# Kernel optimization log

Hardware: AMD Instinct MI355X
Metric: run time of the kernel (lower is better)

## Reference

```python
import jax, jax.numpy as jnp
import numpy as np

N = 20000      # atoms
E = 320000     # edges
G = 16         # graphs
NEL = 4        # chemical elements
M0 = 64        # 0e channels
M1 = 32        # 1o channels
NB = 8         # Bessel basis
L = 2          # conv layers
HID = 64       # radial MLP hidden
RMAX = 4.0
RIN = RMAX - 0.5
NNB = 16.0     # n_neighbors normalization


def _bessel(r):
    # Bessel radial embedding with smooth cosine cutoff between RIN and RMAX
    r_safe = jnp.maximum(r, 1e-6)
    n = jnp.arange(1, NB + 1, dtype=r.dtype)
    f = jnp.sqrt(2.0 / RMAX) * jnp.sin(n[None, :] * jnp.pi * r_safe[:, None] / RMAX) / r_safe[:, None]
    t = (r - RIN) / (RMAX - RIN)
    env = jnp.where(r < RIN, 1.0, jnp.where(r > RMAX, 0.0, 0.5 * (jnp.cos(jnp.pi * t) + 1.0)))
    return f * env[:, None]


def _conv(s, v, attrs, sh0, sh1, src, dst, remb, Wscs, Wscv, W1s, W1v, R0, R1, R2, W2s, W2v):
    # self-connection: FC tensor product of node features with scalar species attrs
    sc_s = jnp.einsum('ni,ne,ieo->no', s, attrs, Wscs) / np.sqrt(M0 * NEL)    # [N, M0+M1]
    sc_v = jnp.einsum('nic,ne,ieo->noc', v, attrs, Wscv) / np.sqrt(M1 * NEL)  # [N, M1, 3]
    # irrep-wise linear (channel mixing)
    s1 = s @ W1s / np.sqrt(M0)
    v1 = jnp.einsum('nic,io->noc', v, W1v) / np.sqrt(M1)
    # gather to edges
    se, ve = s1[src], v1[src]
    # radial MLP -> per-edge tensor-product weights (2*M0 + 2*M1 = 192)
    w = jax.nn.silu(remb @ R0 / np.sqrt(NB))
    w = jax.nn.silu(w @ R1 / np.sqrt(HID))
    w = w @ R2 / np.sqrt(HID)
    w1, w2, w3, w4 = w[:, :M0], w[:, M0:2 * M0], w[:, 2 * M0:2 * M0 + M1], w[:, 2 * M0 + M1:]
    # CG tensor product paths (uvu): 0e*0e->0e, 1o*1o->0e, 0e*1o->1o, 1o*0e->1o
    m_s = jnp.concatenate([
        w1 * se * sh0[:, None],
        w4 * jnp.einsum('eic,ec->ei', ve, sh1) / np.sqrt(3.0),
    ], axis=1)                                                   # [E, M0+M1]
    m_v = jnp.concatenate([
        (w2 * se)[:, :, None] * sh1[:, None, :],
        (w3 * sh0[:, None])[:, :, None] * ve,
    ], axis=1)                                                   # [E, M0+M1, 3]
    # scatter-sum aggregation
    a_s = jax.ops.segment_sum(m_s, dst, num_segments=N) / np.sqrt(NNB)
    a_v = jax.ops.segment_sum(m_v, dst, num_segments=N) / np.sqrt(NNB)
    # linear back to hidden irreps (+ gate scalars) and self-connection
    o_s = a_s @ W2s / np.sqrt(M0 + M1) + sc_s                    # [N, M0+M1]
    o_v = jnp.einsum('nic,io->noc', a_v, W2v) / np.sqrt(M0 + M1) + sc_v
    # gate nonlinearity: silu on scalars, silu-gates on vectors
    gate = jax.nn.silu(o_s[:, M0:])
    return jax.nn.silu(o_s[:, :M0]), o_v * gate[:, :, None]


def _forward(nodes, dR, senders, receivers, n_node, W_embed, W_sc_s, W_sc_v, W_l1_s, W_l1_v,
             Wr0, Wr1, Wr2, W_l2_s, W_l2_v, W_en1, W_en2, W_mag1, W_mag2,
             scale_occ, shift_occ, energy_scale, energy_shift):
    r = jnp.linalg.norm(dR, axis=-1)
    u = dR / jnp.maximum(r, 1e-6)[:, None]
    sh0 = jnp.ones_like(r)                 # Y0 (component norm)
    sh1 = np.sqrt(3.0) * u                 # Y1 (component norm)
    remb = _bessel(r)                      # [E, NB]
    s = nodes @ W_embed / np.sqrt(NEL)     # initial scalar embedding
    v = jnp.zeros((N, M1, 3), dtype=s.dtype)
    for l in range(L):
        s, v = _conv(s, v, nodes, sh0, sh1, senders, receivers, remb,
                     W_sc_s[l], W_sc_v[l], W_l1_s[l], W_l1_v[l],
                     Wr0[l], Wr1[l], Wr2[l], W_l2_s[l], W_l2_v[l])
    # energy readout
    h_en = s @ W_en1 / np.sqrt(M0)
    atomic = h_en @ W_en2 / np.sqrt(M0 // 2)
    atomic = energy_scale * atomic + energy_shift
    gidx = jnp.repeat(jnp.arange(G), n_node, total_repeat_length=N)
    energy = jax.ops.segment_sum(atomic, gidx, num_segments=G)   # [G, 1]
    # magnetization readout
    h_mag = s @ W_mag1 / np.sqrt(M0)
    mags = h_mag @ W_mag2 / np.sqrt(M0 // 2)                     # [N, 2]
    mags = (nodes[:, :-1] @ scale_occ) * mags + (nodes[:, :-1] @ shift_occ)
    return energy, mags


def setup_inputs() -> dict:
    key = jax.random.key(0)
    ks = jax.random.split(key, 30)
    f = jnp.float32
    inp = {
        'nodes': jax.random.uniform(ks[0], (N, NEL), dtype=f),
        'dR': jax.random.normal(ks[1], (E, 3), dtype=f),
        'senders': jax.random.randint(ks[2], (E,), 0, N, dtype=jnp.int32),
        'receivers': jax.random.randint(ks[3], (E,), 0, N, dtype=jnp.int32),
        'n_node': jnp.full((G,), N // G, dtype=jnp.int32),
        'W_embed': jax.random.normal(ks[4], (NEL, M0), dtype=f),
        'W_sc_s': jax.random.normal(ks[5], (L, M0, NEL, M0 + M1), dtype=f),
        'W_sc_v': jax.random.normal(ks[6], (L, M1, NEL, M1), dtype=f),
        'W_l1_s': jax.random.normal(ks[7], (L, M0, M0), dtype=f),
        'W_l1_v': jax.random.normal(ks[8], (L, M1, M1), dtype=f),
        'Wr0': jax.random.normal(ks[9], (L, NB, HID), dtype=f),
        'Wr1': jax.random.normal(ks[10], (L, HID, HID), dtype=f),
        'Wr2': jax.random.normal(ks[11], (L, HID, 2 * M0 + 2 * M1), dtype=f),
        'W_l2_s': jax.random.normal(ks[12], (L, M0 + M1, M0 + M1), dtype=f),
        'W_l2_v': jax.random.normal(ks[13], (L, M0 + M1, M1), dtype=f),
        'W_en1': jax.random.normal(ks[14], (M0, M0 // 2), dtype=f),
        'W_en2': jax.random.normal(ks[15], (M0 // 2, 1), dtype=f),
        'W_mag1': jax.random.normal(ks[16], (M0, M0 // 2), dtype=f),
        'W_mag2': jax.random.normal(ks[17], (M0 // 2, 2), dtype=f),
        'scale_occ': jax.random.uniform(ks[18], (NEL - 1, 2), dtype=f),
        'shift_occ': jax.random.normal(ks[19], (NEL - 1, 2), dtype=f),
        'energy_scale': jnp.ones((), dtype=f),
        'energy_shift': jnp.zeros((), dtype=f),
    }
    return inp


def reference(nodes, dR, senders, receivers, n_node, W_embed, W_sc_s, W_sc_v, W_l1_s, W_l1_v,
              Wr0, Wr1, Wr2, W_l2_s, W_l2_v, W_en1, W_en2, W_mag1, W_mag2,
              scale_occ, shift_occ, energy_scale, energy_shift):
    return _forward(nodes, dR, senders, receivers, n_node, W_embed, W_sc_s, W_sc_v, W_l1_s, W_l1_v,
                    Wr0, Wr1, Wr2, W_l2_s, W_l2_v, W_en1, W_en2, W_mag1, W_mag2,
                    scale_occ, shift_occ, energy_scale, energy_shift)
```

## Files before the change

### kernel.cpp

```cpp
#include <hip/hip_runtime.h>
#include <hip/hip_fp16.h>
#include <math.h>

#define NN 20000
#define NE 320000
#define NG 16
#define ECAP 48

typedef _Float16 f16x2 __attribute__((ext_vector_type(2)));
typedef _Float16 f16x8 __attribute__((ext_vector_type(8)));
typedef float    f32x4 __attribute__((ext_vector_type(4)));

__device__ __forceinline__ float dot2f(f16x2 a, f16x2 b, float c){
#if defined(__has_builtin)
#if __has_builtin(__builtin_amdgcn_fdot2)
  return __builtin_amdgcn_fdot2(a, b, c, false);
#else
  return c + (float)a.x*(float)b.x + (float)a.y*(float)b.y;
#endif
#else
  return c + (float)a.x*(float)b.x + (float)a.y*(float)b.y;
#endif
}

__device__ __forceinline__ f16x2 pack2f(float a, float b){
  f16x2 r; r.x = (_Float16)a; r.y = (_Float16)b; return r;
}

__device__ __forceinline__ float silu_f(float x){ return x / (1.0f + __expf(-x)); }

__device__ __forceinline__ void bessel8(const float* __restrict__ dR, int e, float* rb){
  float x = dR[3*e+0], y = dR[3*e+1], z = dR[3*e+2];
  float r = sqrtf(x*x + y*y + z*z);
  float rs = fmaxf(r, 1e-6f);
  float inv = 1.0f / rs;
  float env;
  if (r < 3.5f) env = 1.0f;
  else if (r > 4.0f) env = 0.0f;
  else {
    float t = (r - 3.5f) * 2.0f;
    env = 0.5f * (cosf(3.14159265358979323846f * t) + 1.0f);
  }
  float c = 0.7071067811865476f * inv * env;
  #pragma unroll
  for (int k=0;k<8;k++){
    float arg = (float)(k+1) * 0.7853981633974483f * rs;
    rb[k] = c * sinf(arg);
  }
}

__global__ void k_geom(const float* __restrict__ dR, float* __restrict__ sh1){
  int e = blockIdx.x*256 + threadIdx.x;
  if (e >= NE) return;
  float x = dR[3*e+0], y = dR[3*e+1], z = dR[3*e+2];
  float r = sqrtf(x*x + y*y + z*z);
  float inv = 1.0f / fmaxf(r, 1e-6f);
  const float SQ3 = 1.7320508075688772f;
  sh1[3*e+0] = SQ3 * x * inv;
  sh1[3*e+1] = SQ3 * y * inv;
  sh1[3*e+2] = SQ3 * z * inv;
}

__global__ void k_prep(const float* __restrict__ dR, const int* __restrict__ senders,
                       const int* __restrict__ perm,
                       float* __restrict__ sh1, float* __restrict__ dRp,
                       int* __restrict__ sendp){
  int p = blockIdx.x*256 + threadIdx.x;
  if (p >= NE) return;
  int e = perm[p];
  float x = dR[3*e+0], y = dR[3*e+1], z = dR[3*e+2];
  dRp[3*p+0] = x; dRp[3*p+1] = y; dRp[3*p+2] = z;
  float r = sqrtf(x*x + y*y + z*z);
  float inv = 1.0f / fmaxf(r, 1e-6f);
  const float SQ3 = 1.7320508075688772f;
  sh1[3*p+0] = SQ3 * x * inv;
  sh1[3*p+1] = SQ3 * y * inv;
  sh1[3*p+2] = SQ3 * z * inv;
  sendp[p] = senders[e];
}

__global__ void k_wt(const float* __restrict__ Wscs, const float* __restrict__ Wscv,
                     float* __restrict__ Wst, float* __restrict__ Wvt){
  int idx = blockIdx.x*256 + threadIdx.x;
  if (idx < 49152){
    int l = idx/24576, r = idx - l*24576;
    int i = r/384; int rem = r - i*384; int e = rem/96; int o = rem - e*96;
    Wst[l*24576 + i*384 + o*4 + e] = Wscs[idx];
  } else if (idx < 49152 + 8192){
    int k = idx - 49152;
    int l = k/4096, r = k - l*4096;
    int i = r/128; int rem = r - i*128; int e = rem/32; int op = rem - e*32;
    Wvt[l*4096 + i*128 + op*4 + e] = Wscv[idx];
  }
}

__global__ void k_embed(const float* __restrict__ nodes, const float* __restrict__ W,
                        float* __restrict__ s){
  int idx = blockIdx.x*256 + threadIdx.x;
  int n = idx>>6, o = idx&63;
  float a = nodes[n*4+0]*W[o] + nodes[n*4+1]*W[64+o]
          + nodes[n*4+2]*W[128+o] + nodes[n*4+3]*W[192+o];
  s[idx] = 0.5f*a;
}

__global__ void k_hist(const int* __restrict__ receivers, int* __restrict__ cnt){
  int e = blockIdx.x*256 + threadIdx.x;
  if (e < NE) atomicAdd(&cnt[receivers[e]], 1);
}

__global__ void k_scan(const int* __restrict__ cnt, int* __restrict__ row, int* __restrict__ cur){
  __shared__ int lsum[1024];
  int t = threadIdx.x;
  int base = t*20;
  int local[20];
  int s = 0;
  #pragma unroll
  for (int i=0;i<20;i++){
    int idx = base+i;
    int v = (idx<NN) ? cnt[idx] : 0;
    local[i] = s; s += v;
  }
  lsum[t] = s; __syncthreads();
  for (int off=1; off<1024; off<<=1){
    int v = (t>=off) ? lsum[t-off] : 0;
    __syncthreads();
    lsum[t] += v;
    __syncthreads();
  }
  int pre = (t>0) ? lsum[t-1] : 0;
  #pragma unroll
  for (int i=0;i<20;i++){
    int idx = base+i;
    if (idx<NN){ int r = pre+local[i]; row[idx]=r; cur[idx]=r; }
  }
  if (t==1023) row[NN] = lsum[1023];
}

__global__ void k_scatter(const int* __restrict__ receivers, int* __restrict__ cur,
                          int* __restrict__ perm){
  int e = blockIdx.x*256 + threadIdx.x;
  if (e < NE){
    int d = receivers[e];
    int p = atomicAdd(&cur[d], 1);
    perm[p] = e;
  }
}

__global__ void k_node(const float* __restrict__ s, const float* __restrict__ v,
                       const float* __restrict__ attrs,
                       const float* __restrict__ W1s, const float* __restrict__ W1v,
                       const float* __restrict__ Wscst, const float* __restrict__ Wscvt,
                       __half* __restrict__ s1, __half* __restrict__ v1,
                       float* __restrict__ scs, float* __restrict__ scv){
  __shared__ float ls[16][64];
  __shared__ float lv[16][96];
  __shared__ float la[16][4];
  int tid = threadIdx.x;
  int nb = blockIdx.x*16;
  for (int i=tid;i<1024;i+=256) ls[i>>6][i&63] = s[(size_t)(nb+(i>>6))*64 + (i&63)];
  for (int i=tid;i<1536;i+=256){ int j=i/96, q=i-96*j; lv[j][q] = v[(size_t)(nb+j)*96+q]; }
  if (tid<64) la[tid>>2][tid&3] = attrs[(nb+(tid>>2))*4 + (tid&3)];
  __syncthreads();
  int w = tid>>6, q = tid&63;
  int jb = w*4;
  float laj[4][4];
  #pragma unroll
  for (int j=0;j<4;j++)
    #pragma unroll
    for (int e=0;e<4;e++) laj[j][e] = la[jb+j][e];

  {
    float acc[4] = {0,0,0,0};
    for (int i=0;i<64;i++){
      float wv = W1s[i*64+q];
      #pragma unroll
      for (int j=0;j<4;j++) acc[j] = fmaf(ls[jb+j][i], wv, acc[j]);
    }
    #pragma unroll
    for (int j=0;j<4;j++) s1[(size_t)(nb+jb+j)*64+q] = __float2half(acc[j]*0.125f);
  }
  #pragma unroll 1
  for (int o=q;o<96;o+=64){
    float t0[4]={0,0,0,0}, t1[4]={0,0,0,0}, t2[4]={0,0,0,0}, t3[4]={0,0,0,0};
    for (int i=0;i<64;i++){
      float4 wv4 = *(const float4*)(Wscst + i*384 + o*4);
      #pragma unroll
      for (int j=0;j<4;j++){
        float sv = ls[jb+j][i];
        t0[j] = fmaf(sv, wv4.x, t0[j]);
        t1[j] = fmaf(sv, wv4.y, t1[j]);
        t2[j] = fmaf(sv, wv4.z, t2[j]);
        t3[j] = fmaf(sv, wv4.w, t3[j]);
      }
    }
    #pragma unroll
    for (int j=0;j<4;j++){
      float acc = t0[j]*laj[j][0] + t1[j]*laj[j][1]
                + t2[j]*laj[j][2] + t3[j]*laj[j][3];
      scs[(size_t)(nb+jb+j)*96+o] = acc*0.0625f;
    }
  }
  #pragma unroll 1
  for (int f=q;f<96;f+=64){
    int op=f/3, c=f-3*op;
    float acc[4] = {0,0,0,0};
    for (int i=0;i<32;i++){
      float wv = W1v[i*32+op];
      #pragma unroll
      for (int j=0;j<4;j++) acc[j] = fmaf(lv[jb+j][i*3+c], wv, acc[j]);
    }
    #pragma unroll
    for (int j=0;j<4;j++) v1[(size_t)(nb+jb+j)*96+f] = __float2half(acc[j]*0.17677669529663687f);
  }
  #pragma unroll 1
  for (int f=q;f<96;f+=64){
    int op=f/3, c=f-3*op;
    float t0[4]={0,0,0,0}, t1[4]={0,0,0,0}, t2[4]={0,0,0,0}, t3[4]={0,0,0,0};
    for (int i=0;i<32;i++){
      float4 wv4 = *(const float4*)(Wscvt + i*128 + op*4);
      #pragma unroll
      for (int j=0;j<4;j++){
        float vv = lv[jb+j][i*3+c];
        t0[j] = fmaf(vv, wv4.x, t0[j]);
        t1[j] = fmaf(vv, wv4.y, t1[j]);
        t2[j] = fmaf(vv, wv4.z, t2[j]);
        t3[j] = fmaf(vv, wv4.w, t3[j]);
      }
    }
    #pragma unroll
    for (int j=0;j<4;j++){
      float acc = t0[j]*laj[j][0] + t1[j]*laj[j][1]
                + t2[j]*laj[j][2] + t3[j]*laj[j][3];
      scv[(size_t)(nb+jb+j)*96+f] = acc*0.08838834764831845f;
    }
  }
}

#define R2S 196
#define HT2S 68
__launch_bounds__(256, 4)
__global__ void k_edgew(const float* __restrict__ dRp,
                        const int* __restrict__ row, int n0, int n1, int cap,
                        const float* __restrict__ R0, const float* __restrict__ R1,
                        const float* __restrict__ R2,
                        __half* __restrict__ wbuf){
  __shared__ __align__(16) f16x2 hT2[32*HT2S];
  __shared__ __align__(16) float r0s[512];
  __shared__ __align__(16) f16x2 wgt2[32*R2S];
  int tid = threadIdx.x;
  int p0 = row[n0], p1 = row[n1];
  int vmax = p1 - p0; if (vmax > cap) vmax = cap;
  int tbase = blockIdx.x*64;
  if (tbase >= vmax) return;
  int vcnt = vmax - tbase; if (vcnt > 64) vcnt = 64;

  if (tid < 128) ((float4*)r0s)[tid] = ((const float4*)R0)[tid];
  for (int i=tid; i<2048; i+=256){
    int kp = i>>6, j = i&63;
    wgt2[kp*HT2S + j] = pack2f(R1[(2*kp)*64 + j], R1[(2*kp+1)*64 + j]);
  }
  float* hTf = (float*)hT2;
  if (tid < 64){
    float rbv[8];
    if (tid < vcnt){
      bessel8(dRp, p0 + tbase + tid, rbv);
    } else {
      #pragma unroll
      for (int k=0;k<8;k++) rbv[k]=0.0f;
    }
    #pragma unroll
    for (int k=0;k<8;k++) hTf[k*HT2S + tid] = rbv[k];
  }
  __syncthreads();

  int eg = tid & 15;
  int jg = tid >> 4, j0 = jg*4;

  float rb[8][4];
  {
    const float4* hTf4 = (const float4*)hTf;
    #pragma unroll
    for (int k=0;k<8;k++){
      float4 v = hTf4[k*17 + eg];
      rb[k][0]=v.x; rb[k][1]=v.y; rb[k][2]=v.z; rb[k][3]=v.w;
    }
  }
  float a[4][4];
  #pragma unroll
  for (int j=0;j<4;j++)
    #pragma unroll
    for (int e=0;e<4;e++) a[j][e]=0.0f;
  {
    const float4* r0s4 = (const float4*)r0s;
    #pragma unroll
    for (int k=0;k<8;k++){
      float4 w = r0s4[k*16 + jg];
      float wj[4] = {w.x,w.y,w.z,w.w};
      #pragma unroll
      for (int j=0;j<4;j++)
        #pragma unroll
        for (int e=0;e<4;e++) a[j][e] = fmaf(rb[k][e], wj[j], a[j][e]);
    }
  }
  #pragma unroll
  for (int j=0;j<4;j++)
    #pragma unroll
    for (int e=0;e<4;e++) a[j][e] = silu_f(a[j][e]*0.3535533905932738f);
  __syncthreads();
  int e0 = eg*4;
  #pragma unroll
  for (int jp=0;jp<2;jp++){
    union {uint4 u; f16x2 h[4];} U;
    #pragma unroll
    for (int e=0;e<4;e++) U.h[e] = pack2f(a[2*jp][e], a[2*jp+1][e]);
    *(uint4*)(hT2 + (j0/2 + jp)*HT2S + e0) = U.u;
  }
  __syncthreads();

  {
    int wv = tid >> 6;
    int ln = tid & 63;
    int col = ln & 15;
    int quad = ln >> 4;
    const unsigned int* hT2u = (const unsigned int*)hT2;
    const unsigned int* wgt2u = (const unsigned int*)wgt2;
    union { uint4 u; f16x8 v; } A0, A1;
    int jA = 16*wv + col;
    A0.u.x = wgt2u[(4*quad+0)*HT2S + jA];
    A0.u.y = wgt2u[(4*quad+1)*HT2S + jA];
    A0.u.z = wgt2u[(4*quad+2)*HT2S + jA];
    A0.u.w = wgt2u[(4*quad+3)*HT2S + jA];
    A1.u.x = wgt2u[(16+4*quad+0)*HT2S + jA];
    A1.u.y = wgt2u[(16+4*quad+1)*HT2S + jA];
    A1.u.z = wgt2u[(16+4*quad+2)*HT2S + jA];
    A1.u.w = wgt2u[(16+4*quad+3)*HT2S + jA];
    f32x4 accB[4];
    #pragma unroll
    for (int nt=0; nt<4; nt++){
      union { uint4 u; f16x8 v; } B0, B1;
      int eB = 16*nt + col;
      B0.u.x = hT2u[(4*quad+0)*HT2S + eB];
      B0.u.y = hT2u[(4*quad+1)*HT2S + eB];
      B0.u.z = hT2u[(4*quad+2)*HT2S + eB];
      B0.u.w = hT2u[(4*quad+3)*HT2S + eB];
      B1.u.x = hT2u[(16+4*quad+0)*HT2S + eB];
      B1.u.y = hT2u[(16+4*quad+1)*HT2S + eB];
      B1.u.z = hT2u[(16+4*quad+2)*HT2S + eB];
      B1.u.w = hT2u[(16+4*quad+3)*HT2S + eB];
      f32x4 acc = {0.0f,0.0f,0.0f,0.0f};
      acc = __builtin_amdgcn_mfma_f32_16x16x32_f16(A0.v, B0.v, acc, 0, 0, 0);
      acc = __builtin_amdgcn_mfma_f32_16x16x32_f16(A1.v, B1.v, acc, 0, 0, 0);
      accB[nt] = acc;
    }
    __syncthreads();
    #pragma unroll
    for (int nt=0; nt<4; nt++){
      float h0 = silu_f(accB[nt][0]*0.125f);
      float h1v = silu_f(accB[nt][1]*0.125f);
      float h2v = silu_f(accB[nt][2]*0.125f);
      float h3v = silu_f(accB[nt][3]*0.125f);
      hT2[(8*wv + 2*quad + 0)*HT2S + 16*nt + col] = pack2f(h0, h1v);
      hT2[(8*wv + 2*quad + 1)*HT2S + 16*nt + col] = pack2f(h2v, h3v);
    }
  }
  for (int i=tid; i<6144; i+=256){
    int kp = i/192, o = i-192*kp;
    wgt2[kp*R2S + o] = pack2f(R2[(2*kp)*192 + o], R2[(2*kp+1)*192 + o]);
  }
  __syncthreads();

  {
    int wv = tid >> 6;
    int ln = tid & 63;
    int col = ln & 15;
    int quad = ln >> 4;
    const unsigned int* hT2u = (const unsigned int*)hT2;
    const unsigned int* wgt2u = (const unsigned int*)wgt2;
    int eA = 16*wv + col;
    union { uint4 u; f16x8 v; } A0, A1;
    A0.u.x = hT2u[(4*quad+0)*HT2S + eA];
    A0.u.y = hT2u[(4*quad+1)*HT2S + eA];
    A0.u.z = hT2u[(4*quad+2)*HT2S + eA];
    A0.u.w = hT2u[(4*quad+3)*HT2S + eA];
    A1.u.x = hT2u[(16+4*quad+0)*HT2S + eA];
    A1.u.y = hT2u[(16+4*quad+1)*HT2S + eA];
    A1.u.z = hT2u[(16+4*quad+2)*HT2S + eA];
    A1.u.w = hT2u[(16+4*quad+3)*HT2S + eA];
    int erow = 16*wv + 4*quad;
    float accs[12][4];
    #pragma unroll
    for (int ot=0; ot<12; ot++){
      int o = 16*ot + col;
      union { uint4 u; f16x8 v; } B0, B1;
      B0.u.x = wgt2u[(4*quad+0)*R2S + o];
      B0.u.y = wgt2u[(4*quad+1)*R2S + o];
      B0.u.z = wgt2u[(4*quad+2)*R2S + o];
      B0.u.w = wgt2u[(4*quad+3)*R2S + o];
      B1.u.x = wgt2u[(16+4*quad+0)*R2S + o];
      B1.u.y = wgt2u[(16+4*quad+1)*R2S + o];
      B1.u.z = wgt2u[(16+4*quad+2)*R2S + o];
      B1.u.w = wgt2u[(16+4*quad+3)*R2S + o];
      f32x4 acc = {0.0f,0.0f,0.0f,0.0f};
      acc = __builtin_amdgcn_mfma_f32_16x16x32_f16(A0.v, B0.v, acc, 0, 0, 0);
      acc = __builtin_amdgcn_mfma_f32_16x16x32_f16(A1.v, B1.v, acc, 0, 0, 0);
      accs[ot][0] = acc[0]; accs[ot][1] = acc[1];
      accs[ot][2] = acc[2]; accs[ot][3] = acc[3];
    }
    __syncthreads();
    __half* wtile = (__half*)wgt2;
    #pragma unroll
    for (int ot=0; ot<12; ot++){
      #pragma unroll
      for (int r=0;r<4;r++)
        wtile[(erow+r)*196 + 16*ot + col] = __float2half(accs[ot][r]);
    }
    __syncthreads();
    for (int i=tid; i<3072; i+=256){
      int e = i/48, c = i-48*e;
      if (e < vcnt){
        uint2 val = *(const uint2*)(wtile + e*196 + c*4);
        *((uint2*)(wbuf + (size_t)(tbase+e)*192) + c) = val;
      }
    }
  }
}

__launch_bounds__(128, 8)
__global__ void k_gather(const __half* __restrict__ wbuf,
                         const int* __restrict__ row, const int* __restrict__ sendp,
                         const float* __restrict__ sh1,
                         const __half* __restrict__ s1, const __half* __restrict__ v1,
                         int n0, int cap,
                         float* __restrict__ a_s, float* __restrict__ a_v){
  __shared__ int   srcs[ECAP];
  __shared__ float sh1r[ECAP*3];
  int n = n0 + blockIdx.x;
  int t = threadIdx.x;
  int pc0 = row[n0];
  int p0 = row[n], p1 = row[n+1];
  int pmax = pc0 + cap; if (p1 > pmax) p1 = pmax;
  float acc0 = 0.0f, acc1 = 0.0f, acc2 = 0.0f;

  for (int base = p0; base < p1; base += ECAP){
    int bc = p1 - base; if (bc > ECAP) bc = ECAP;
    __syncthreads();
    if (t < bc){
      srcs[t] = sendp[base + t];
      sh1r[3*t+0] = sh1[3*(base+t)+0];
      sh1r[3*t+1] = sh1[3*(base+t)+1];
      sh1r[3*t+2] = sh1[3*(base+t)+2];
    }
    __syncthreads();
    const __half* wb = wbuf + (size_t)(base - pc0)*192;
    if (t < 64){
      for (int j=0;j<bc;j++)
        acc0 = fmaf(__half2float(wb[j*192 + t]),
                    __half2float(s1[(size_t)srcs[j]*64 + t]), acc0);
    } else if (t < 96){
      int i = t-64;
      for (int j=0;j<bc;j++){
        const __half* vr = v1 + (size_t)srcs[j]*96 + 3*i;
        float dv = __half2float(vr[0])*sh1r[j*3+0]
                 + __half2float(vr[1])*sh1r[j*3+1]
                 + __half2float(vr[2])*sh1r[j*3+2];
        acc0 = fmaf(__half2float(wb[j*192 + 160 + i]), dv, acc0);
      }
    } else {
      int idx = t-96; int op = idx/3; int c = idx-3*op;
      for (int j=0;j<bc;j++)
        acc0 = fmaf(__half2float(wb[j*192 + 64 + op]) *
                    __half2float(s1[(size_t)srcs[j]*64 + op]),
                    sh1r[j*3+c], acc0);
    }
    {
      int idx = t+32; int op = idx/3; int c = idx-3*op;
      for (int j=0;j<bc;j++)
        acc1 = fmaf(__half2float(wb[j*192 + 64 + op]) *
                    __half2float(s1[(size_t)srcs[j]*64 + op]),
                    sh1r[j*3+c], acc1);
    }
    {
      int idx = t+160; int op = idx/3; int c = idx-3*op;
      if (op < 64){
        for (int j=0;j<bc;j++)
          acc2 = fmaf(__half2float(wb[j*192 + 64 + op]) *
                      __half2float(s1[(size_t)srcs[j]*64 + op]),
                      sh1r[j*3+c], acc2);
      } else {
        int i = op-64;
        for (int j=0;j<bc;j++)
          acc2 = fmaf(__half2float(wb[j*192 + 128 + i]),
                      __half2float(v1[(size_t)srcs[j]*96 + 3*i + c]), acc2);
      }
    }
  }

  if (t < 64){
    a_s[(size_t)n*96 + t] = 0.03125f*acc0;
  } else if (t < 96){
    a_s[(size_t)n*96 + t] = 0.018042195912175807f*acc0;
  } else {
    a_v[(size_t)n*288 + (t-96)] = 0.03125f*acc0;
  }
  a_v[(size_t)n*288 + (t+32)]  = 0.03125f*acc1;
  a_v[(size_t)n*288 + (t+160)] = 0.03125f*acc2;
}

__device__ __forceinline__ void mlp_h2(const float* __restrict__ R0,
                                       const float* lR1, const float rb[8],
                                       float h2[64]){
  float h1[64];
  #pragma unroll
  for (int j=0;j<64;j+=4){
    float a0=0,a1=0,a2=0,a3=0;
    #pragma unroll
    for (int k=0;k<8;k++){
      float r = rb[k];
      const float* wp = R0 + k*64 + j;
      a0 = fmaf(r, wp[0], a0); a1 = fmaf(r, wp[1], a1);
      a2 = fmaf(r, wp[2], a2); a3 = fmaf(r, wp[3], a3);
    }
    h1[j+0]=silu_f(a0*0.3535533905932738f);
    h1[j+1]=silu_f(a1*0.3535533905932738f);
    h1[j+2]=silu_f(a2*0.3535533905932738f);
    h1[j+3]=silu_f(a3*0.3535533905932738f);
  }
  #pragma unroll
  for (int j=0;j<64;j+=4){
    float a0=0,a1=0,a2=0,a3=0;
    #pragma unroll
    for (int k=0;k<64;k++){
      float h = h1[k];
      float4 w4 = *(const float4*)(lR1 + k*64 + j);
      a0 = fmaf(h,w4.x,a0); a1 = fmaf(h,w4.y,a1);
      a2 = fmaf(h,w4.z,a2); a3 = fmaf(h,w4.w,a3);
    }
    h2[j+0]=silu_f(a0*0.125f);
    h2[j+1]=silu_f(a1*0.125f);
    h2[j+2]=silu_f(a2*0.125f);
    h2[j+3]=silu_f(a3*0.125f);
  }
}

__launch_bounds__(256, 2)
__global__ void k_edge(const float* __restrict__ dR, const float* __restrict__ sh1,
                       const int* __restrict__ senders, const int* __restrict__ receivers,
                       const __half* __restrict__ s1, const __half* __restrict__ v1,
                       const float* __restrict__ R0, const float* __restrict__ R1,
                       const float* __restrict__ R2,
                       float* __restrict__ a_s, float* __restrict__ a_v){
  __shared__ __align__(16) float lR1[64*64];
  __shared__ __align__(16) float lR2[64*192];
  int tid = threadIdx.x;
  for (int i=tid;i<4096;i+=256)  lR1[i]=R1[i];
  for (int i=tid;i<12288;i+=256) lR2[i]=R2[i];
  __syncthreads();
  int e = blockIdx.x*256 + tid;
  float rb[8];
  bessel8(dR, e, rb);
  float h2[64];
  mlp_h2(R0, lR1, rb, h2);
  int src = senders[e], dst = receivers[e];
  float sx=sh1[3*e+0], sy=sh1[3*e+1], sz=sh1[3*e+2];
  const __half* srow = s1 + (size_t)src*64;
  const __half* vrow = v1 + (size_t)src*96;
  float* asr = a_s + (size_t)dst*96;
  float* avr = a_v + (size_t)dst*288;
  #pragma unroll 1
  for (int o=0;o<64;o+=4){
    float w10=0,w11=0,w12=0,w13=0, w20=0,w21=0,w22=0,w23=0;
    #pragma unroll
    for (int k=0;k<64;k++){
      float h = h2[k];
      float4 wa = *(const float4*)(lR2 + k*192 + o);
      float4 wb = *(const float4*)(lR2 + k*192 + 64 + o);
      w10=fmaf(h,wa.x,w10); w11=fmaf(h,wa.y,w11); w12=fmaf(h,wa.z,w12); w13=fmaf(h,wa.w,w13);
      w20=fmaf(h,wb.x,w20); w21=fmaf(h,wb.y,w21); w22=fmaf(h,wb.z,w22); w23=fmaf(h,wb.w,w23);
    }
    float sev[4] = {__half2float(srow[o+0]), __half2float(srow[o+1]),
                    __half2float(srow[o+2]), __half2float(srow[o+3])};
    float w1a[4] = {w10,w11,w12,w13};
    float w2a[4] = {w20,w21,w22,w23};
    #pragma unroll
    for (int u=0;u<4;u++){
      atomicAdd(asr+o+u, 0.03125f*w1a[u]*sev[u]);
      float m = 0.03125f*w2a[u]*sev[u];
      atomicAdd(avr+(o+u)*3+0, m*sx);
      atomicAdd(avr+(o+u)*3+1, m*sy);
      atomicAdd(avr+(o+u)*3+2, m*sz);
    }
  }
  #pragma unroll 1
  for (int i0=0;i0<32;i0+=4){
    float w30=0,w31=0,w32=0,w33=0, w40=0,w41=0,w42=0,w43=0;
    #pragma unroll
    for (int k=0;k<64;k++){
      float h = h2[k];
      float4 wa = *(const float4*)(lR2 + k*192 + 128 + i0);
      float4 wb = *(const float4*)(lR2 + k*192 + 160 + i0);
      w30=fmaf(h,wa.x,w30); w31=fmaf(h,wa.y,w31); w32=fmaf(h,wa.z,w32); w33=fmaf(h,wa.w,w33);
      w40=fmaf(h,wb.x,w40); w41=fmaf(h,wb.y,w41); w42=fmaf(h,wb.z,w42); w43=fmaf(h,wb.w,w43);
    }
    float w3a[4] = {w30,w31,w32,w33};
    float w4a[4] = {w40,w41,w42,w43};
    #pragma unroll
    for (int u=0;u<4;u++){
      int i = i0+u;
      float vx=__half2float(vrow[3*i+0]), vy=__half2float(vrow[3*i+1]), vz=__half2float(vrow[3*i+2]);
      float dv = vx*sx + vy*sy + vz*sz;
      atomicAdd(asr+64+i, 0.018042195912175807f*w4a[u]*dv);
      float m3 = 0.03125f*w3a[u];
      atomicAdd(avr+(64+i)*3+0, m3*vx);
      atomicAdd(avr+(64+i)*3+1, m3*vy);
      atomicAdd(avr+(64+i)*3+2, m3*vz);
    }
  }
}

__launch_bounds__(256, 4)
__global__ void k_out(const float* __restrict__ a_s, const float* __restrict__ a_v,
                      const float* __restrict__ scs, const float* __restrict__ scv,
                      const float* __restrict__ W2s, const float* __restrict__ W2v,
                      float* __restrict__ s_out, float* __restrict__ v_out){
  __shared__ float las[16][96];
  __shared__ float lav[16][288];
  __shared__ float los[16][96];
  int tid = threadIdx.x;
  int nb = blockIdx.x*16;
  for (int i=tid;i<1536;i+=256){ int j=i/96,  q=i-96*j;  las[j][q] = a_s[(size_t)(nb+j)*96 +q]; }
  for (int i=tid;i<4608;i+=256){ int j=i/288, q=i-288*j; lav[j][q] = a_v[(size_t)(nb+j)*288+q]; }
  __syncthreads();
  int w = tid>>6, q = tid&63;
  int jb = w*4;

  #pragma unroll 1
  for (int o=q; o<96; o+=64){
    float acc[4] = {0,0,0,0};
    for (int i=0;i<96;i++){
      float wv = W2s[i*96+o];
      #pragma unroll
      for (int j=0;j<4;j++) acc[j] = fmaf(las[jb+j][i], wv, acc[j]);
    }
    #pragma unroll
    for (int j=0;j<4;j++)
      los[jb+j][o] = acc[j]*0.10206207261596575f + scs[(size_t)(nb+jb+j)*96+o];
  }
  __syncthreads();

  #pragma unroll
  for (int j=0;j<4;j++) s_out[(size_t)(nb+jb+j)*64+q] = silu_f(los[jb+j][q]);

  #pragma unroll 1
  for (int f=q; f<96; f+=64){
    int op=f/3, c=f-3*op;
    float acc[4] = {0,0,0,0};
    for (int i=0;i<96;i++){
      float wv = W2v[i*32+op];
      #pragma unroll
      for (int j=0;j<4;j++) acc[j] = fmaf(lav[jb+j][i*3+c], wv, acc[j]);
    }
    #pragma unroll
    for (int j=0;j<4;j++){
      float ov = acc[j]*0.10206207261596575f + scv[(size_t)(nb+jb+j)*96+f];
      float g = silu_f(los[jb+j][64+op]);
      v_out[(size_t)(nb+jb+j)*96+f] = ov*g;
    }
  }
}

__global__ void k_final(const float* __restrict__ s, const float* __restrict__ nodes,
                        const int* __restrict__ n_node,
                        const float* __restrict__ Wen1, const float* __restrict__ Wen2,
                        const float* __restrict__ Wm1, const float* __restrict__ Wm2,
                        const float* __restrict__ scale_occ, const float* __restrict__ shift_occ,
                        const float* __restrict__ escale, const float* __restrict__ eshift,
                        float* __restrict__ out){
  __shared__ float eacc[NG];
  __shared__ int goff[NG+1];
  int tid = threadIdx.x;
  if (tid < NG) eacc[tid] = 0.0f;
  if (tid == 0){
    int c = 0; goff[0] = 0;
    for (int g=0; g<NG; g++){ c += n_node[g]; goff[g+1] = c; }
  }
  __syncthreads();
  int n = blockIdx.x*256 + tid;
  if (n < NN){
    float sv[64];
    #pragma unroll
    for (int i=0;i<64;i++) sv[i]=s[(size_t)n*64+i];
    float en=0.0f, m0=0.0f, m1=0.0f;
    #pragma unroll 1
    for (int jj=0;jj<32;jj++){
      float he=0.0f, hm=0.0f;
      #pragma unroll
      for (int i=0;i<64;i++){
        he = fmaf(sv[i], Wen1[i*32+jj], he);
        hm = fmaf(sv[i], Wm1[i*32+jj], hm);
      }
      he *= 0.125f; hm *= 0.125f;
      en = fmaf(he, Wen2[jj], en);
      m0 = fmaf(hm, Wm2[jj*2+0], m0);
      m1 = fmaf(hm, Wm2[jj*2+1], m1);
    }
    const float INVS32 = 0.17677669529663687f;
    en *= INVS32; m0 *= INVS32; m1 *= INVS32;
    en = escale[0]*en + eshift[0];
    int g = 0;
    for (int gg=0; gg<NG; gg++) if (n >= goff[gg+1]) g = gg+1;
    atomicAdd(&eacc[g], en);
    float nx=nodes[n*4+0], ny=nodes[n*4+1], nz=nodes[n*4+2];
    float sc0 = nx*scale_occ[0] + ny*scale_occ[2] + nz*scale_occ[4];
    float sc1 = nx*scale_occ[1] + ny*scale_occ[3] + nz*scale_occ[5];
    float sf0 = nx*shift_occ[0] + ny*shift_occ[2] + nz*shift_occ[4];
    float sf1 = nx*shift_occ[1] + ny*shift_occ[3] + nz*shift_occ[5];
    out[16 + n*2 + 0] = sc0*m0 + sf0;
    out[16 + n*2 + 1] = sc1*m1 + sf1;
  }
  __syncthreads();
  if (tid < NG) atomicAdd(&out[tid], eacc[tid]);
}

extern "C" void kernel_launch(void* const* d_in, const int* in_sizes, int n_in,
                              void* d_out, int out_size, void* d_ws, size_t ws_size,
                              hipStream_t stream){
  const float* nodes   = (const float*)d_in[0];
  const float* dR      = (const float*)d_in[1];
  const int*  senders  = (const int*)d_in[2];
  const int*  receivers= (const int*)d_in[3];
  const int*  n_node   = (const int*)d_in[4];
  const float* W_embed = (const float*)d_in[5];
  const float* W_sc_s  = (const float*)d_in[6];
  const float* W_sc_v  = (const float*)d_in[7];
  const float* W_l1_s  = (const float*)d_in[8];
  const float* W_l1_v  = (const float*)d_in[9];
  const float* Wr0     = (const float*)d_in[10];
  const float* Wr1     = (const float*)d_in[11];
  const float* Wr2     = (const float*)d_in[12];
  const float* W_l2_s  = (const float*)d_in[13];
  const float* W_l2_v  = (const float*)d_in[14];
  const float* W_en1   = (const float*)d_in[15];
  const float* W_en2   = (const float*)d_in[16];
  const float* W_mag1  = (const float*)d_in[17];
  const float* W_mag2  = (const float*)d_in[18];
  const float* scale_occ = (const float*)d_in[19];
  const float* shift_occ = (const float*)d_in[20];
  const float* escale  = (const float*)d_in[21];
  const float* eshift  = (const float*)d_in[22];
  float* out = (float*)d_out;
  float* ws  = (float*)d_ws;

  float*  sh1  = ws + 0;
  float*  sA   = ws + 960000;
  float*  vA   = ws + 2240000;
  __half* s1h  = (__half*)(ws + 4160000);
  __half* v1h  = (__half*)(ws + 4800000);
  float*  dRp  = ws + 5760000;
  int*    sendp= (int*)(ws + 6720000);
  float*  Wst  = ws + 7040000;
  float*  Wvt  = ws + 7089152;
  float*  scs  = ws + 7360000;
  float*  scv  = ws + 9280000;
  float*  a_s  = ws + 11200000;
  float*  a_v  = ws + 13120000;
  int*    cnt  = (int*)(ws + 18880000);
  int*    row  = (int*)(ws + 18900000);
  int*    cur  = (int*)(ws + 18920004);
  int*    perm = (int*)(ws + 18940004);
  __half* wbuf = (__half*)(ws + 19260008);

  size_t wsf = ws_size / 4;
  size_t cap_edges = (wsf > 19260008) ? ((wsf - 19260008)*4) / 384 : 0;
  if (cap_edges > 128) cap_edges -= 64;
  const bool fast = cap_edges >= 4096;
  int cap = (int)((cap_edges > (size_t)NE) ? (size_t)NE + 8192 : cap_edges);
  int npc;
  if (cap_edges > (size_t)NE){
    npc = NN;
  } else {
    npc = (int)(cap / 20); if (npc < 1) npc = 1; if (npc > NN) npc = NN;
  }
  int nchunk = (NN + npc - 1) / npc;

  hipMemsetAsync(vA, 0, (size_t)NN*96*sizeof(float), stream);
  hipMemsetAsync(out, 0, 16*sizeof(float), stream);

  k_embed<<<5000, 256, 0, stream>>>(nodes, W_embed, sA);
  k_wt<<<225, 256, 0, stream>>>(W_sc_s, W_sc_v, Wst, Wvt);

  if (fast){
    hipMemsetAsync(cnt, 0, NN*sizeof(int), stream);
    k_hist<<<1250, 256, 0, stream>>>(receivers, cnt);
    k_scan<<<1, 1024, 0, stream>>>(cnt, row, cur);
    k_scatter<<<1250, 256, 0, stream>>>(receivers, cur, perm);
    k_prep<<<1250, 256, 0, stream>>>(dR, senders, perm, sh1, dRp, sendp);
  } else {
    k_geom<<<1250, 256, 0, stream>>>(dR, sh1);
  }

  for (int l=0; l<2; l++){
    k_node<<<1250, 256, 0, stream>>>(sA, vA, nodes,
                                     W_l1_s + l*4096, W_l1_v + l*1024,
                                     Wst + l*24576, Wvt + l*4096,
                                     s1h, v1h, scs, scv);
    if (fast){
      for (int ck=0; ck<nchunk; ck++){
        int n0 = ck*npc;
        int n1 = n0 + npc; if (n1 > NN) n1 = NN;
        int cover = (n1-n0)*17 + 4096; if (cover > cap) cover = cap;
        k_edgew<<<(cover+63)/64, 256, 0, stream>>>(dRp, row, n0, n1, cap,
                                       Wr0 + l*512, Wr1 + l*4096, Wr2 + l*12288, wbuf);
        k_gather<<<n1-n0, 128, 0, stream>>>(wbuf, row, sendp, sh1, s1h, v1h,
                                            n0, cap, a_s, a_v);
      }
    } else {
      hipMemsetAsync(a_s, 0, (size_t)NN*384*sizeof(float), stream);
      k_edge<<<1250, 256, 0, stream>>>(dR, sh1, senders, receivers, s1h, v1h,
                                       Wr0 + l*512, Wr1 + l*4096, Wr2 + l*12288,
                                       a_s, a_v);
    }
    k_out<<<1250, 256, 0, stream>>>(a_s, a_v, scs, scv,
                                    W_l2_s + l*9216, W_l2_v + l*3072,
                                    sA, vA);
  }
  k_final<<<79, 256, 0, stream>>>(sA, nodes, n_node, W_en1, W_en2, W_mag1, W_mag2,
                                  scale_occ, shift_occ, escale, eshift, out);
}
```

Before: 665.5 us.

## Make edge-weight MLP kernel persistent and keep MLP weights resident in LDS

k_edgew becomes a grid-stride persistent kernel, capped at 768 blocks, that loads R1 and R2 into shared memory once per block and reuses them across many 64-edge tiles. This removes the repeated per-tile weight staging from global memory. R1 gets its own LDS buffer, which raises shared memory use, so launch bounds drop from 4 to 3 blocks per CU. The final output now goes straight from MFMA accumulators to global memory with 2-byte stores, instead of being staged through an LDS tile and written with vectorized copies. Those stores may coalesce less well.

```diff
diff --git a/kernel.cpp b/kernel.cpp
--- a/kernel.cpp
+++ b/kernel.cpp
@@ -238,7 +238,7 @@
 
 #define R2S 196
 #define HT2S 68
-__launch_bounds__(256, 4)
+__launch_bounds__(256, 3)
 __global__ void k_edgew(const float* __restrict__ dRp,
                         const int* __restrict__ row, int n0, int n1, int cap,
                         const float* __restrict__ R0, const float* __restrict__ R1,
@@ -246,180 +246,168 @@
                         __half* __restrict__ wbuf){
   __shared__ __align__(16) f16x2 hT2[32*HT2S];
   __shared__ __align__(16) float r0s[512];
+  __shared__ __align__(16) f16x2 wgt1[32*HT2S];
   __shared__ __align__(16) f16x2 wgt2[32*R2S];
   int tid = threadIdx.x;
   int p0 = row[n0], p1 = row[n1];
   int vmax = p1 - p0; if (vmax > cap) vmax = cap;
-  int tbase = blockIdx.x*64;
-  if (tbase >= vmax) return;
-  int vcnt = vmax - tbase; if (vcnt > 64) vcnt = 64;
+  int ntiles = (vmax + 63) >> 6;
 
   if (tid < 128) ((float4*)r0s)[tid] = ((const float4*)R0)[tid];
   for (int i=tid; i<2048; i+=256){
     int kp = i>>6, j = i&63;
-    wgt2[kp*HT2S + j] = pack2f(R1[(2*kp)*64 + j], R1[(2*kp+1)*64 + j]);
-  }
-  float* hTf = (float*)hT2;
-  if (tid < 64){
-    float rbv[8];
-    if (tid < vcnt){
-      bessel8(dRp, p0 + tbase + tid, rbv);
-    } else {
-      #pragma unroll
-      for (int k=0;k<8;k++) rbv[k]=0.0f;
-    }
-    #pragma unroll
-    for (int k=0;k<8;k++) hTf[k*HT2S + tid] = rbv[k];
-  }
-  __syncthreads();
-
-  int eg = tid & 15;
-  int jg = tid >> 4, j0 = jg*4;
-
-  float rb[8][4];
-  {
-    const float4* hTf4 = (const float4*)hTf;
-    #pragma unroll
-    for (int k=0;k<8;k++){
-      float4 v = hTf4[k*17 + eg];
-      rb[k][0]=v.x; rb[k][1]=v.y; rb[k][2]=v.z; rb[k][3]=v.w;
-    }
-  }
-  float a[4][4];
-  #pragma unroll
-  for (int j=0;j<4;j++)
-    #pragma unroll
-    for (int e=0;e<4;e++) a[j][e]=0.0f;
-  {
-    const float4* r0s4 = (const float4*)r0s;
-    #pragma unroll
-    for (int k=0;k<8;k++){
-      float4 w = r0s4[k*16 + jg];
-      float wj[4] = {w.x,w.y,w.z,w.w};
-      #pragma unroll
-      for (int j=0;j<4;j++)
-        #pragma unroll
-        for (int e=0;e<4;e++) a[j][e] = fmaf(rb[k][e], wj[j], a[j][e]);
-    }
-  }
-  #pragma unroll
-  for (int j=0;j<4;j++)
-    #pragma unroll
-    for (int e=0;e<4;e++) a[j][e] = silu_f(a[j][e]*0.3535533905932738f);
-  __syncthreads();
-  int e0 = eg*4;
-  #pragma unroll
-  for (int jp=0;jp<2;jp++){
-    union {uint4 u; f16x2 h[4];} U;
-    #pragma unroll
-    for (int e=0;e<4;e++) U.h[e] = pack2f(a[2*jp][e], a[2*jp+1][e]);
-    *(uint4*)(hT2 + (j0/2 + jp)*HT2S + e0) = U.u;
-  }
-  __syncthreads();
-
-  {
-    int wv = tid >> 6;
-    int ln = tid & 63;
-    int col = ln & 15;
-    int quad = ln >> 4;
-    const unsigned int* hT2u = (const unsigned int*)hT2;
-    const unsigned int* wgt2u = (const unsigned int*)wgt2;
-    union { uint4 u; f16x8 v; } A0, A1;
-    int jA = 16*wv + col;
-    A0.u.x = wgt2u[(4*quad+0)*HT2S + jA];
-    A0.u.y = wgt2u[(4*quad+1)*HT2S + jA];
-    A0.u.z = wgt2u[(4*quad+2)*HT2S + jA];
-    A0.u.w = wgt2u[(4*quad+3)*HT2S + jA];
-    A1.u.x = wgt2u[(16+4*quad+0)*HT2S + jA];
-    A1.u.y = wgt2u[(16+4*quad+1)*HT2S + jA];
-    A1.u.z = wgt2u[(16+4*quad+2)*HT2S + jA];
-    A1.u.w = wgt2u[(16+4*quad+3)*HT2S + jA];
-    f32x4 accB[4];
-    #pragma unroll
-    for (int nt=0; nt<4; nt++){
-      union { uint4 u; f16x8 v; } B0, B1;
-      int eB = 16*nt + col;
-      B0.u.x = hT2u[(4*quad+0)*HT2S + eB];
-      B0.u.y = hT2u[(4*quad+1)*HT2S + eB];
-      B0.u.z = hT2u[(4*quad+2)*HT2S + eB];
-      B0.u.w = hT2u[(4*quad+3)*HT2S + eB];
-      B1.u.x = hT2u[(16+4*quad+0)*HT2S + eB];
-      B1.u.y = hT2u[(16+4*quad+1)*HT2S + eB];
-      B1.u.z = hT2u[(16+4*quad+2)*HT2S + eB];
-      B1.u.w = hT2u[(16+4*quad+3)*HT2S + eB];
-      f32x4 acc = {0.0f,0.0f,0.0f,0.0f};
-      acc = __builtin_amdgcn_mfma_f32_16x16x32_f16(A0.v, B0.v, acc, 0, 0, 0);
-      acc = __builtin_amdgcn_mfma_f32_16x16x32_f16(A1.v, B1.v, acc, 0, 0, 0);
-      accB[nt] = acc;
-    }
-    __syncthreads();
-    #pragma unroll
-    for (int nt=0; nt<4; nt++){
-      float h0 = silu_f(accB[nt][0]*0.125f);
-      float h1v = silu_f(accB[nt][1]*0.125f);
-      float h2v = silu_f(accB[nt][2]*0.125f);
-      float h3v = silu_f(accB[nt][3]*0.125f);
-      hT2[(8*wv + 2*quad + 0)*HT2S + 16*nt + col] = pack2f(h0, h1v);
-      hT2[(8*wv + 2*quad + 1)*HT2S + 16*nt + col] = pack2f(h2v, h3v);
-    }
+    wgt1[kp*HT2S + j] = pack2f(R1[(2*kp)*64 + j], R1[(2*kp+1)*64 + j]);
   }
   for (int i=tid; i<6144; i+=256){
     int kp = i/192, o = i-192*kp;
     wgt2[kp*R2S + o] = pack2f(R2[(2*kp)*192 + o], R2[(2*kp+1)*192 + o]);
   }
-  __syncthreads();
-
-  {
-    int wv = tid >> 6;
-    int ln = tid & 63;
-    int col = ln & 15;
-    int quad = ln >> 4;
-    const unsigned int* hT2u = (const unsigned int*)hT2;
-    const unsigned int* wgt2u = (const unsigned int*)wgt2;
-    int eA = 16*wv + col;
-    union { uint4 u; f16x8 v; } A0, A1;
-    A0.u.x = hT2u[(4*quad+0)*HT2S + eA];
-    A0.u.y = hT2u[(4*quad+1)*HT2S + eA];
-    A0.u.z = hT2u[(4*quad+2)*HT2S + eA];
-    A0.u.w = hT2u[(4*quad+3)*HT2S + eA];
-    A1.u.x = hT2u[(16+4*quad+0)*HT2S + eA];
-    A1.u.y = hT2u[(16+4*quad+1)*HT2S + eA];
-    A1.u.z = hT2u[(16+4*quad+2)*HT2S + eA];
-    A1.u.w = hT2u[(16+4*quad+3)*HT2S + eA];
-    int erow = 16*wv + 4*quad;
-    float accs[12][4];
-    #pragma unroll
-    for (int ot=0; ot<12; ot++){
-      int o = 16*ot + col;
-      union { uint4 u; f16x8 v; } B0, B1;
-      B0.u.x = wgt2u[(4*quad+0)*R2S + o];
-      B0.u.y = wgt2u[(4*quad+1)*R2S + o];
-      B0.u.z = wgt2u[(4*quad+2)*R2S + o];
-      B0.u.w = wgt2u[(4*quad+3)*R2S + o];
-      B1.u.x = wgt2u[(16+4*quad+0)*R2S + o];
-      B1.u.y = wgt2u[(16+4*quad+1)*R2S + o];
-      B1.u.z = wgt2u[(16+4*quad+2)*R2S + o];
-      B1.u.w = wgt2u[(16+4*quad+3)*R2S + o];
-      f32x4 acc = {0.0f,0.0f,0.0f,0.0f};
-      acc = __builtin_amdgcn_mfma_f32_16x16x32_f16(A0.v, B0.v, acc, 0, 0, 0);
-      acc = __builtin_amdgcn_mfma_f32_16x16x32_f16(A1.v, B1.v, acc, 0, 0, 0);
-      accs[ot][0] = acc[0]; accs[ot][1] = acc[1];
-      accs[ot][2] = acc[2]; accs[ot][3] = acc[3];
-    }
+
+  int eg = tid & 15, e0 = eg*4;
+  int jg = tid >> 4, j0 = jg*4;
+  int wv = tid >> 6;
+  int ln = tid & 63;
+  int col = ln & 15;
+  int quad = ln >> 4;
+
+  for (int tile = blockIdx.x; tile < ntiles; tile += gridDim.x){
+    int tbase = tile*64;
+    int vcnt = vmax - tbase; if (vcnt > 64) vcnt = 64;
+
     __syncthreads();
-    __half* wtile = (__half*)wgt2;
-    #pragma unroll
-    for (int ot=0; ot<12; ot++){
-      #pragma unroll
-      for (int r=0;r<4;r++)
-        wtile[(erow+r)*196 + 16*ot + col] = __float2half(accs[ot][r]);
+    float* hTf = (float*)hT2;
+    if (tid < 64){
+      float rbv[8];
+      if (tid < vcnt){
+        bessel8(dRp, p0 + tbase + tid, rbv);
+      } else {
+        #pragma unroll
+        for (int k=0;k<8;k++) rbv[k]=0.0f;
+      }
+      #pragma unroll
+      for (int k=0;k<8;k++) hTf[k*HT2S + tid] = rbv[k];
     }
     __syncthreads();
-    for (int i=tid; i<3072; i+=256){
-      int e = i/48, c = i-48*e;
-      if (e < vcnt){
-        uint2 val = *(const uint2*)(wtile + e*196 + c*4);
-        *((uint2*)(wbuf + (size_t)(tbase+e)*192) + c) = val;
+
+    float rb[8][4];
+    {
+      const float4* hTf4 = (const float4*)hTf;
+      #pragma unroll
+      for (int k=0;k<8;k++){
+        float4 v = hTf4[k*17 + eg];
+        rb[k][0]=v.x; rb[k][1]=v.y; rb[k][2]=v.z; rb[k][3]=v.w;
+      }
+    }
+    float a[4][4];
+    #pragma unroll
+    for (int j=0;j<4;j++)
+      #pragma unroll
+      for (int e=0;e<4;e++) a[j][e]=0.0f;
+    {
+      const float4* r0s4 = (const float4*)r0s;
+      #pragma unroll
+      for (int k=0;k<8;k++){
+        float4 w = r0s4[k*16 + jg];
+        float wj[4] = {w.x,w.y,w.z,w.w};
+        #pragma unroll
+        for (int j=0;j<4;j++)
+          #pragma unroll
+          for (int e=0;e<4;e++) a[j][e] = fmaf(rb[k][e], wj[j], a[j][e]);
+      }
+    }
+    #pragma unroll
+    for (int j=0;j<4;j++)
+      #pragma unroll
+      for (int e=0;e<4;e++) a[j][e] = silu_f(a[j][e]*0.3535533905932738f);
+    __syncthreads();
+    #pragma unroll
+    for (int jp=0;jp<2;jp++){
+      union {uint4 u; f16x2 h[4];} U;
+      #pragma unroll
+      for (int e=0;e<4;e++) U.h[e] = pack2f(a[2*jp][e], a[2*jp+1][e]);
+      *(uint4*)(hT2 + (j0/2 + jp)*HT2S + e0) = U.u;
+    }
+    __syncthreads();
+
+    {
+      const unsigned int* hT2u = (const unsigned int*)hT2;
+      const unsigned int* wgt1u = (const unsigned int*)wgt1;
+      union { uint4 u; f16x8 v; } A0, A1;
+      int jA = 16*wv + col;
+      A0.u.x = wgt1u[(4*quad+0)*HT2S + jA];
+      A0.u.y = wgt1u[(4*quad+1)*HT2S + jA];
+      A0.u.z = wgt1u[(4*quad+2)*HT2S + jA];
+      A0.u.w = wgt1u[(4*quad+3)*HT2S + jA];
+      A1.u.x = wgt1u[(16+4*quad+0)*HT2S + jA];
+      A1.u.y = wgt1u[(16+4*quad+1)*HT2S + jA];
+      A1.u.z = wgt1u[(16+4*quad+2)*HT2S + jA];
+      A1.u.w = wgt1u[(16+4*quad+3)*HT2S + jA];
+      f32x4 accB[4];
+      #pragma unroll
+      for (int nt=0; nt<4; nt++){
+        union { uint4 u; f16x8 v; } B0, B1;
+        int eB = 16*nt + col;
+        B0.u.x = hT2u[(4*quad+0)*HT2S + eB];
+        B0.u.y = hT2u[(4*quad+1)*HT2S + eB];
+        B0.u.z = hT2u[(4*quad+2)*HT2S + eB];
+        B0.u.w = hT2u[(4*quad+3)*HT2S + eB];
+        B1.u.x = hT2u[(16+4*quad+0)*HT2S + eB];
+        B1.u.y = hT2u[(16+4*quad+1)*HT2S + eB];
+        B1.u.z = hT2u[(16+4*quad+2)*HT2S + eB];
+        B1.u.w = hT2u[(16+4*quad+3)*HT2S + eB];
+        f32x4 acc = {0.0f,0.0f,0.0f,0.0f};
+        acc = __builtin_amdgcn_mfma_f32_16x16x32_f16(A0.v, B0.v, acc, 0, 0, 0);
+        acc = __builtin_amdgcn_mfma_f32_16x16x32_f16(A1.v, B1.v, acc, 0, 0, 0);
+        accB[nt] = acc;
+      }
+      __syncthreads();
+      #pragma unroll
+      for (int nt=0; nt<4; nt++){
+        float h0 = silu_f(accB[nt][0]*0.125f);
+        float h1v = silu_f(accB[nt][1]*0.125f);
+        float h2v = silu_f(accB[nt][2]*0.125f);
+        float h3v = silu_f(accB[nt][3]*0.125f);
+        hT2[(8*wv + 2*quad + 0)*HT2S + 16*nt + col] = pack2f(h0, h1v);
+        hT2[(8*wv + 2*quad + 1)*HT2S + 16*nt + col] = pack2f(h2v, h3v);
+      }
+    }
+    __syncthreads();
+
+    {
+      const unsigned int* hT2u = (const unsigned int*)hT2;
+      const unsigned int* wgt2u = (const unsigned int*)wgt2;
+      int eA = 16*wv + col;
+      union { uint4 u; f16x8 v; } A0, A1;
+      A0.u.x = hT2u[(4*quad+0)*HT2S + eA];
+      A0.u.y = hT2u[(4*quad+1)*HT2S + eA];
+      A0.u.z = hT2u[(4*quad+2)*HT2S + eA];
+      A0.u.w = hT2u[(4*quad+3)*HT2S + eA];
+      A1.u.x = hT2u[(16+4*quad+0)*HT2S + eA];
+      A1.u.y = hT2u[(16+4*quad+1)*HT2S + eA];
+      A1.u.z = hT2u[(16+4*quad+2)*HT2S + eA];
+      A1.u.w = hT2u[(16+4*quad+3)*HT2S + eA];
+      int erow = 16*wv + 4*quad;
+      #pragma unroll
+      for (int ot=0; ot<12; ot++){
+        int o = 16*ot + col;
+        union { uint4 u; f16x8 v; } B0, B1;
+        B0.u.x = wgt2u[(4*quad+0)*R2S + o];
+        B0.u.y = wgt2u[(4*quad+1)*R2S + o];
+        B0.u.z = wgt2u[(4*quad+2)*R2S + o];
+        B0.u.w = wgt2u[(4*quad+3)*R2S + o];
+        B1.u.x = wgt2u[(16+4*quad+0)*R2S + o];
+        B1.u.y = wgt2u[(16+4*quad+1)*R2S + o];
+        B1.u.z = wgt2u[(16+4*quad+2)*R2S + o];
+        B1.u.w = wgt2u[(16+4*quad+3)*R2S + o];
+        f32x4 acc = {0.0f,0.0f,0.0f,0.0f};
+        acc = __builtin_amdgcn_mfma_f32_16x16x32_f16(A0.v, B0.v, acc, 0, 0, 0);
+        acc = __builtin_amdgcn_mfma_f32_16x16x32_f16(A1.v, B1.v, acc, 0, 0, 0);
+        #pragma unroll
+        for (int r=0;r<4;r++){
+          int eib = erow + r;
+          if (eib < vcnt)
+            wbuf[(size_t)(tbase+eib)*192 + o] = __float2half(acc[r]);
+        }
       }
     }
   }
@@ -808,7 +796,9 @@
         int n0 = ck*npc;
         int n1 = n0 + npc; if (n1 > NN) n1 = NN;
         int cover = (n1-n0)*17 + 4096; if (cover > cap) cover = cap;
-        k_edgew<<<(cover+63)/64, 256, 0, stream>>>(dRp, row, n0, n1, cap,
+        int ntile_ub = (cover+63)/64;
+        int grid = ntile_ub < 768 ? ntile_ub : 768;
+        k_edgew<<<grid, 256, 0, stream>>>(dRp, row, n0, n1, cap,
                                        Wr0 + l*512, Wr1 + l*4096, Wr2 + l*12288, wbuf);
         k_gather<<<n1-n0, 128, 0, stream>>>(wbuf, row, sendp, sh1, s1h, v1h,
                                             n0, cap, a_s, a_v);
```

Result: faster. 649.3 us (-2.4%).
